# Performance work log

Measured on AMD Instinct MI355X. Metric: run time of the kernel, lower is better.

The kernel has to match this reference:

```python
import jax, jax.numpy as jnp
import numpy as np

H_DIM = 768
NUM_HEADS = 12
HEAD_DIM = H_DIM // NUM_HEADS
ROPE_BASE = 10000.0


def rope_cos_sin(seq_len, dim):
    inv_freq = 1.0 / (ROPE_BASE ** (jnp.arange(0, dim, 2, dtype=jnp.float32) / dim))
    t = jnp.arange(seq_len, dtype=jnp.float32)
    freqs = jnp.outer(t, inv_freq)              # [seq, dim/2]
    emb = jnp.concatenate([freqs, freqs], axis=-1)  # [seq, dim]
    return jnp.cos(emb), jnp.sin(emb)


def rotate_half(x):
    x1, x2 = jnp.split(x, 2, axis=-1)
    return jnp.concatenate([-x2, x1], axis=-1)


def setup_inputs() -> dict:
    key = jax.random.key(0)
    ks = jax.random.split(key, 9)
    s = 1.0 / np.sqrt(H_DIM)
    inp = {
        'x': jax.random.normal(ks[0], (2, 8, 1024, H_DIM), dtype=jnp.float32),
        'Wq': jax.random.normal(ks[1], (H_DIM, H_DIM), dtype=jnp.float32) * s,
        'bq': jnp.zeros((H_DIM,), dtype=jnp.float32),
        'Wk': jax.random.normal(ks[2], (H_DIM, H_DIM), dtype=jnp.float32) * s,
        'bk': jnp.zeros((H_DIM,), dtype=jnp.float32),
        'Wv': jax.random.normal(ks[3], (H_DIM, H_DIM), dtype=jnp.float32) * s,
        'bv': jnp.zeros((H_DIM,), dtype=jnp.float32),
        'Wo': jax.random.normal(ks[4], (H_DIM, H_DIM), dtype=jnp.float32) * s,
        'bo': jnp.zeros((H_DIM,), dtype=jnp.float32),
        'mask': jnp.ones((2, 8, 1, 1, 1024), dtype=jnp.int32),
    }
    return inp


def reference(x, Wq, bq, Wk, bk, Wv, bv, Wo, bo, mask):
    b, r, s, d = x.shape
    H, D = NUM_HEADS, HEAD_DIM

    def proj(W, bvec):
        # [b,r,s,d] -> [b,r,H,s,D]
        y = x @ W + bvec
        return y.reshape(b, r, s, H, D).transpose(0, 1, 3, 2, 4)

    q = proj(Wq, bq)
    k = proj(Wk, bk)
    v = proj(Wv, bv)

    cos, sin = rope_cos_sin(s, D)   # [s, D]
    cos = cos[None, None, None]     # broadcast over b,r,H
    sin = sin[None, None, None]
    q = q * cos + rotate_half(q) * sin
    k = k * cos + rotate_half(k) * sin

    scores = jnp.einsum('brhqd,brhkd->brhqk', q, k) / jnp.sqrt(jnp.float32(D))
    scores = jnp.where(mask == 0, -jnp.inf, scores)
    probs = jax.nn.softmax(scores, axis=-1)  # dropout is identity in eval
    out = jnp.einsum('brhqk,brhkd->brhqd', probs, v)
    out = out.transpose(0, 1, 3, 2, 4).reshape(b, r, s, d)
    return out @ Wo + bo
```

## Files before the change

kernel.cpp:

```cpp
#include <hip/hip_runtime.h>


#define M_TOT 16384
#define DM    768
#define NH    12
#define HD    64
#define SEQ   1024

typedef __attribute__((ext_vector_type(8))) __bf16 bf16x8;
typedef __attribute__((ext_vector_type(4))) __bf16 bf16x4;
typedef __attribute__((ext_vector_type(4))) short s16x4;
typedef __attribute__((ext_vector_type(4))) float  f32x4;

static __device__ __forceinline__ unsigned short f2b(float f) {
  unsigned u = __builtin_bit_cast(unsigned, f);
  u += 0x7FFFu + ((u >> 16) & 1u);
  return (unsigned short)(u >> 16);
}
static __device__ __forceinline__ float b2f(unsigned short s) {
  unsigned u = ((unsigned)s) << 16;
  return __builtin_bit_cast(float, u);
}
static __device__ __forceinline__ unsigned cvt_pk_bf16(float lo, float hi) {
  unsigned d;
  asm("v_cvt_pk_bf16_f32 %0, %1, %2" : "=v"(d) : "v"(lo), "v"(hi));
  return d;
}

static __device__ __forceinline__ f32x4 mfma16(uint2 a, uint2 b, f32x4 c) {
#if __has_builtin(__builtin_amdgcn_mfma_f32_16x16x16_bf16)
  union U { uint2 u; bf16x4 v; } A, B;
  A.u = a; B.u = b;
  return __builtin_amdgcn_mfma_f32_16x16x16_bf16(A.v, B.v, c, 0, 0, 0);
#else
  union U { uint2 u; s16x4 v; } A, B;
  A.u = a; B.u = b;
  return __builtin_amdgcn_mfma_f32_16x16x16bf16_1k(A.v, B.v, c, 0, 0, 0);
#endif
}

static __device__ __forceinline__ void gl_lds16(const void* g, void* l) {
  __builtin_amdgcn_global_load_lds(
      (const __attribute__((address_space(1))) unsigned*)g,
      (__attribute__((address_space(3))) unsigned*)l, 16, 0, 0);
}

static __device__ __forceinline__ int swz_src(int c) {
  return ((c >> 3) << 6) + (((c & 7) ^ ((c >> 3) & 7)) << 3);
}
static __device__ __forceinline__ int swz_rd(int row, int col16) {
  return (row << 6) + ((col16 ^ (row & 7)) << 3);
}

__global__ void cvt_x(const float* __restrict__ x, unsigned short* __restrict__ xb) {
  const int n4 = M_TOT * DM / 4;
  for (int i = blockIdx.x * blockDim.x + threadIdx.x; i < n4; i += gridDim.x * blockDim.x) {
    float4 v = ((const float4*)x)[i];
    ushort4 o;
    o.x = f2b(v.x); o.y = f2b(v.y); o.z = f2b(v.z); o.w = f2b(v.w);
    ((ushort4*)xb)[i] = o;
  }
}

__global__ void prep(const float* __restrict__ Wq, const float* __restrict__ Wk,
                     const float* __restrict__ Wv, const float* __restrict__ Wo,
                     unsigned short* __restrict__ Wt,
                     float* __restrict__ cosT, float* __restrict__ sinT,
                     const float* __restrict__ bq, const float* __restrict__ bk,
                     const float* __restrict__ bv, float* __restrict__ bcat) {
  __shared__ float T[64][65];
  const int bid = blockIdx.x;
  const int t = threadIdx.x;
  if (bid < 576) {
    const int wsel = bid / 144, r144 = bid % 144;
    const int k0 = (r144 % 12) * 64, n0 = (r144 / 12) * 64;
    const float* W = wsel == 0 ? Wq : wsel == 1 ? Wk : wsel == 2 ? Wv : Wo;
#pragma unroll
    for (int p = 0; p < 16; ++p) {
      int e = p * 256 + t, r = e >> 6, c = e & 63;
      T[r][c] = W[(size_t)(k0 + r) * DM + n0 + c];
    }
    __syncthreads();
    unsigned short* dst = Wt + (size_t)wsel * DM * DM;
#pragma unroll
    for (int p = 0; p < 16; ++p) {
      int e = p * 256 + t, r = e >> 6, c = e & 63;
      dst[(size_t)(n0 + r) * DM + k0 + c] = f2b(T[c][r]);
    }
  } else if (bid < 704) {
    int i = (bid - 576) * 256 + t;
    int s = i >> 5, j = i & 31;
    float inv = powf(10000.0f, -(float)j * (1.0f / 32.0f));
    float ang = (float)s * inv;
    cosT[i] = cosf(ang);
    sinT[i] = sinf(ang);
  } else {
    int i = (bid - 704) * 256 + t;
    if (i < 3 * DM)
      bcat[i] = i < DM ? bq[i] : (i < 2 * DM ? bk[i - DM] : bv[i - 2 * DM]);
  }
}

static __device__ __forceinline__ void gemm_core(const unsigned short* __restrict__ A,
                                                 const unsigned short* __restrict__ Bt,
                                                 int m0, int n0, f32x4 acc[4][4],
                                                 char* smem) {
  unsigned short* As = (unsigned short*)smem;
  unsigned short* Bs = As + 128 * 64;
  const int tid = threadIdx.x, lane = tid & 63, w = tid >> 6;
  const int wr = w >> 1, wc = w & 1;
  const int lr = lane & 15, g4 = lane >> 4;

#pragma unroll
  for (int i = 0; i < 4; ++i)
#pragma unroll
    for (int j = 0; j < 4; ++j) acc[i][j] = (f32x4){0.f, 0.f, 0.f, 0.f};

  auto STAGE = [&](int k0) {
#pragma unroll
    for (int p = 0; p < 4; ++p) {
      int cb = p * 256 + w * 64;
      int c = cb + lane;
      const int ro = c >> 3;
      const int co = ((c & 7) ^ (ro & 7)) << 3;
      gl_lds16(A + (size_t)(m0 + ro) * DM + k0 + co, (char*)As + cb * 16);
      gl_lds16(Bt + (size_t)(n0 + ro) * DM + k0 + co, (char*)Bs + cb * 16);
    }
  };

  STAGE(0);
  __syncthreads();

  for (int kt = 0; kt < DM / 64; ++kt) {
    bf16x8 a[4], b[4];
    {
      const int ch = g4;
#pragma unroll
      for (int i = 0; i < 4; ++i) {
        const int row = wr * 64 + i * 16 + lr;
        a[i] = *(const bf16x8*)&As[(row << 6) + ((ch ^ (row & 7)) << 3)];
      }
#pragma unroll
      for (int j = 0; j < 4; ++j) {
        const int row = wc * 64 + j * 16 + lr;
        b[j] = *(const bf16x8*)&Bs[(row << 6) + ((ch ^ (row & 7)) << 3)];
      }
      __builtin_amdgcn_s_setprio(1);
#pragma unroll
      for (int i = 0; i < 4; ++i)
#pragma unroll
        for (int j = 0; j < 4; ++j)
          acc[i][j] = __builtin_amdgcn_mfma_f32_16x16x32_bf16(a[i], b[j], acc[i][j], 0, 0, 0);
      __builtin_amdgcn_s_setprio(0);
    }
    bf16x8 a1[4], b1[4];
    {
      const int ch = 4 + g4;
#pragma unroll
      for (int i = 0; i < 4; ++i) {
        const int row = wr * 64 + i * 16 + lr;
        a1[i] = *(const bf16x8*)&As[(row << 6) + ((ch ^ (row & 7)) << 3)];
      }
#pragma unroll
      for (int j = 0; j < 4; ++j) {
        const int row = wc * 64 + j * 16 + lr;
        b1[j] = *(const bf16x8*)&Bs[(row << 6) + ((ch ^ (row & 7)) << 3)];
      }
    }
    __syncthreads();
    if (kt + 1 < DM / 64) STAGE((kt + 1) * 64);
    __builtin_amdgcn_s_setprio(1);
#pragma unroll
    for (int i = 0; i < 4; ++i)
#pragma unroll
      for (int j = 0; j < 4; ++j)
        acc[i][j] = __builtin_amdgcn_mfma_f32_16x16x32_bf16(a1[i], b1[j], acc[i][j], 0, 0, 0);
    __builtin_amdgcn_s_setprio(0);
    __syncthreads();
  }
}

__global__ __launch_bounds__(256, 4) void gemm_qkv(
    const unsigned short* __restrict__ xb, const unsigned short* __restrict__ Wt,
    const float* __restrict__ bcat, const float* __restrict__ cosT,
    const float* __restrict__ sinT, unsigned short* __restrict__ Qh,
    unsigned short* __restrict__ Kh, unsigned short* __restrict__ Vt) {
  __shared__ alignas(16) char smem[32768];
  const int id = blockIdx.x;
  const int xcdc = id & 7, rem = id >> 3;
  const int y = rem % 18, xc = rem / 18;
  const int xm = xc * 8 + xcdc;
  const int m0 = xm * 128, n0 = y * 128;
  f32x4 acc[4][4];
  gemm_core(xb, Wt, m0, n0, acc, smem);

  const int tid = threadIdx.x, lane = tid & 63, w = tid >> 6;
  const int wr = w >> 1, wc = w & 1;
  const int lr = lane & 15, g4 = lane >> 4;
  const int zone = y / 6;
  const int wcol0 = n0 - zone * DM + wc * 64;
  const int h = wcol0 >> 6;
  const int br = m0 >> 10;
  const int s_base = (m0 & 1023) + wr * 64;

  if (zone == 2) {
    unsigned short* dstb = Vt + ((size_t)(br * NH + h) * HD) * SEQ;
#pragma unroll
    for (int j = 0; j < 4; ++j) {
      const int d = j * 16 + lr;
      const float bv = bcat[n0 + wc * 64 + d];
#pragma unroll
      for (int i = 0; i < 4; ++i) {
        const int s0 = s_base + i * 16 + g4 * 4;
        ushort4 st;
        st.x = f2b(acc[i][j][0] + bv);
        st.y = f2b(acc[i][j][1] + bv);
        st.z = f2b(acc[i][j][2] + bv);
        st.w = f2b(acc[i][j][3] + bv);
        *(ushort4*)&dstb[(size_t)d * SEQ + s0] = st;
      }
    }
  } else {
    const float sc = zone == 0 ? 0.125f * 1.44269504f : 1.0f;
    unsigned short* dstb = (zone ? Kh : Qh) + ((size_t)(br * NH + h) * SEQ) * HD;
    char* Wb = smem + (size_t)w * 8192;
    const int s_q = s_base + lane;
    const int bcol = n0 + wc * 64;

#pragma unroll
    for (int hh = 0; hh < 2; ++hh) {
#pragma unroll
      for (int jj = 0; jj < 2; ++jj) {
        const int jp = hh + jj * 2;
        const float bv = bcat[bcol + jp * 16 + lr];
        const int dslot = jj * 16 + lr;
        const int sub = (dslot & 3) * 4;
        const int ch = dslot >> 2;
#pragma unroll
        for (int i = 0; i < 4; ++i) {
#pragma unroll
          for (int r = 0; r < 4; ++r) {
            const int s_loc = i * 16 + g4 * 4 + r;
            *(float*)(Wb + s_loc * 128 + ((ch ^ (s_loc & 7)) << 4) + sub) =
                (acc[i][jp][r] + bv) * sc;
          }
        }
      }
      unsigned short* drow = dstb + (size_t)s_q * HD + hh * 16;
      const char* Rb = Wb + lane * 128;
      const int lx = lane & 7;
#pragma unroll
      for (int c = 0; c < 4; ++c) {
        f32x4 va = *(const f32x4*)(Rb + ((c ^ lx) << 4));
        f32x4 vb = *(const f32x4*)(Rb + (((c + 4) ^ lx) << 4));
        float4 c4 = *(const float4*)&cosT[s_q * 32 + hh * 16 + c * 4];
        float4 s4 = *(const float4*)&sinT[s_q * 32 + hh * 16 + c * 4];
        uint2 oa, ob;
        oa.x = cvt_pk_bf16(va[0] * c4.x - vb[0] * s4.x, va[1] * c4.y - vb[1] * s4.y);
        oa.y = cvt_pk_bf16(va[2] * c4.z - vb[2] * s4.z, va[3] * c4.w - vb[3] * s4.w);
        ob.x = cvt_pk_bf16(vb[0] * c4.x + va[0] * s4.x, vb[1] * c4.y + va[1] * s4.y);
        ob.y = cvt_pk_bf16(vb[2] * c4.z + va[2] * s4.z, vb[3] * c4.w + va[3] * s4.w);
        *(uint2*)(drow + c * 4)      = oa;
        *(uint2*)(drow + 32 + c * 4) = ob;
      }
    }
  }
}

__global__ __launch_bounds__(256, 4) void gemm_o(const unsigned short* __restrict__ attnb,
                                                 const unsigned short* __restrict__ WtO,
                                                 const float* __restrict__ bo,
                                                 float* __restrict__ out) {
  __shared__ alignas(16) char smem[32768];
  const int id = blockIdx.x;
  const int xcdc = id & 7, rem = id >> 3;
  const int y = rem % 6, xc = rem / 6;
  const int m0 = (xc * 8 + xcdc) * 128, n0 = y * 128;
  f32x4 acc[4][4];
  gemm_core(attnb, WtO, m0, n0, acc, smem);
  const int tid = threadIdx.x, lane = tid & 63, w = tid >> 6;
  const int wr = w >> 1, wc = w & 1;
  const int lr = lane & 15, g4 = lane >> 4;
#pragma unroll
  for (int j = 0; j < 4; ++j) {
    const int col = n0 + wc * 64 + j * 16 + lr;
    const float bv = bo[col];
#pragma unroll
    for (int i = 0; i < 4; ++i) {
      const int rowb = m0 + wr * 64 + i * 16 + g4 * 4;
#pragma unroll
      for (int r = 0; r < 4; ++r)
        out[(size_t)(rowb + r) * DM + col] = acc[i][j][r] + bv;
    }
  }
}

__global__ __launch_bounds__(256) void attn_fwd(const unsigned short* __restrict__ Qh,
                                                const unsigned short* __restrict__ Kh,
                                                const unsigned short* __restrict__ Vt,
                                                const int* __restrict__ mask,
                                                unsigned short* __restrict__ attnb) {
  __shared__ unsigned short Ks[2][64 * 64];
  __shared__ unsigned short Vs[2][64 * 64];
  const int id = blockIdx.x;
  const int xcdc = id & 7, rem = id >> 3;
  const int qp = rem & 7, g = rem >> 3;
  const int brh = g * 8 + xcdc;
  const int br = brh / NH, h = brh - br * NH;
  const int tid = threadIdx.x, lane = tid & 63, w = tid >> 6;
  const int lr = lane & 15, g4 = lane >> 4;

  const unsigned short* Kg = Kh + (size_t)brh * SEQ * HD;
  const unsigned short* Vg = Vt + (size_t)brh * HD * SEQ;
  const int* mrow0 = mask + (size_t)br * SEQ + g4 * 4;

  int4 mi = *(const int4*)&mask[(size_t)br * SEQ + tid * 4];
  const int allLive = __syncthreads_and(mi.x && mi.y && mi.z && mi.w);

#pragma unroll
  for (int p = 0; p < 2; ++p) {
    int cb = p * 256 + w * 64;
    int c = cb + lane;
    gl_lds16(Kg + swz_src(c), (char*)Ks[0] + cb * 16);
    gl_lds16(Vg + (size_t)(c >> 3) * SEQ + (((c & 7) ^ ((c >> 3) & 7)) << 3),
             (char*)Vs[0] + cb * 16);
  }

  const unsigned short* Qg0 =
      Qh + ((size_t)brh * SEQ + qp * 128 + w * 16 + lr) * HD;
  bf16x8 qa0[2], qa1[2];
  qa0[0] = *(const bf16x8*)(Qg0 + g4 * 8);
  qa0[1] = *(const bf16x8*)(Qg0 + 32 + g4 * 8);
  qa1[0] = *(const bf16x8*)(Qg0 + (size_t)64 * HD + g4 * 8);
  qa1[1] = *(const bf16x8*)(Qg0 + (size_t)64 * HD + 32 + g4 * 8);

  f32x4 o0[4], o1[4], lacc0, lacc1;
#pragma unroll
  for (int j = 0; j < 4; ++j) {
    o0[j] = (f32x4){0.f, 0.f, 0.f, 0.f};
    o1[j] = (f32x4){0.f, 0.f, 0.f, 0.f};
  }
  lacc0 = (f32x4){0.f, 0.f, 0.f, 0.f};
  lacc1 = (f32x4){0.f, 0.f, 0.f, 0.f};
  const uint2 ones = {0x3F803F80u, 0x3F803F80u};

  __syncthreads();

  unsigned short* KsC = Ks[0];
  unsigned short* VsC = Vs[0];
  unsigned short* KsN = Ks[1];
  unsigned short* VsN = Vs[1];

  for (int kb = 0; kb < SEQ / 64; ++kb) {
    if (kb + 1 < SEQ / 64) {
#pragma unroll
      for (int p = 0; p < 2; ++p) {
        int cb = p * 256 + w * 64;
        int c = cb + lane;
        gl_lds16(Kg + (size_t)(kb + 1) * 64 * HD + swz_src(c), (char*)KsN + cb * 16);
        gl_lds16(Vg + (size_t)(c >> 3) * SEQ + (kb + 1) * 64 +
                     (((c & 7) ^ ((c >> 3) & 7)) << 3),
                 (char*)VsN + cb * 16);
      }
    }

#pragma unroll
    for (int qi = 0; qi < 2; ++qi) {
      const bf16x8* qa = qi ? qa1 : qa0;
      f32x4* o = qi ? o1 : o0;
      f32x4& lacc = qi ? lacc1 : lacc0;

      f32x4 s4[4];
#pragma unroll
      for (int j = 0; j < 4; ++j) s4[j] = (f32x4){0.f, 0.f, 0.f, 0.f};
      __builtin_amdgcn_s_setprio(1);
#pragma unroll
      for (int kk = 0; kk < 2; ++kk) {
#pragma unroll
        for (int j = 0; j < 4; ++j) {
          bf16x8 kf = *(const bf16x8*)&KsC[swz_rd(j * 16 + lr, kk * 4 + g4)];
          s4[j] = __builtin_amdgcn_mfma_f32_16x16x32_bf16(kf, qa[kk], s4[j], 0, 0, 0);
        }
      }
      __builtin_amdgcn_s_setprio(0);

      if (!allLive) {
        const int* mr = mrow0 + kb * 64;
#pragma unroll
        for (int j = 0; j < 4; ++j) {
          int4 mq = *(const int4*)&mr[j * 16];
          s4[j][0] += mq.x ? 0.f : -3e38f;
          s4[j][1] += mq.y ? 0.f : -3e38f;
          s4[j][2] += mq.z ? 0.f : -3e38f;
          s4[j][3] += mq.w ? 0.f : -3e38f;
        }
      }

      uint2 wb[4];
#pragma unroll
      for (int j = 0; j < 4; ++j) {
        wb[j].x = cvt_pk_bf16(exp2f(s4[j][0]), exp2f(s4[j][1]));
        wb[j].y = cvt_pk_bf16(exp2f(s4[j][2]), exp2f(s4[j][3]));
      }

      __builtin_amdgcn_s_setprio(1);
#pragma unroll
      for (int j = 0; j < 4; ++j) lacc = mfma16(ones, wb[j], lacc);
#pragma unroll
      for (int jj = 0; jj < 4; ++jj) {
        const int row = jj * 16 + lr;
#pragma unroll
        for (int j = 0; j < 4; ++j) {
          const int c8 = j * 4 + g4;
          uint2 av = *(const uint2*)&VsC[(row << 6) + ((((c8 >> 1) ^ (lr & 7))) << 3) +
                                         ((c8 & 1) << 2)];
          o[jj] = mfma16(av, wb[j], o[jj]);
        }
      }
      __builtin_amdgcn_s_setprio(0);
    }

    __syncthreads();
    unsigned short* t;
    t = KsC; KsC = KsN; KsN = t;
    t = VsC; VsC = VsN; VsN = t;
  }

#pragma unroll
  for (int qi = 0; qi < 2; ++qi) {
    f32x4* o = qi ? o1 : o0;
    float l = qi ? lacc1[0] : lacc0[0];
    float inv = l > 0.f ? 1.0f / l : 0.f;
    unsigned short* dst =
        attnb + ((size_t)(br * SEQ + qp * 128 + qi * 64 + w * 16 + lr)) * DM + h * HD;
#pragma unroll
    for (int j = 0; j < 4; ++j) {
      ushort4 st;
      st.x = f2b(o[j][0] * inv);
      st.y = f2b(o[j][1] * inv);
      st.z = f2b(o[j][2] * inv);
      st.w = f2b(o[j][3] * inv);
      *(ushort4*)&dst[j * 16 + g4 * 4] = st;
    }
  }
}

extern "C" void kernel_launch(void* const* d_in, const int* in_sizes, int n_in,
                              void* d_out, int out_size, void* d_ws, size_t ws_size,
                              hipStream_t stream) {
  const float* x  = (const float*)d_in[0];
  const float* Wq = (const float*)d_in[1];
  const float* bq = (const float*)d_in[2];
  const float* Wk = (const float*)d_in[3];
  const float* bk = (const float*)d_in[4];
  const float* Wv = (const float*)d_in[5];
  const float* bv = (const float*)d_in[6];
  const float* Wo = (const float*)d_in[7];
  const float* bo = (const float*)d_in[8];
  const int* mask = (const int*)d_in[9];
  float* out = (float*)d_out;

  const size_t OFF_XB   = 0;
  const size_t OFF_WT   = 25165824;
  const size_t OFF_COS  = 29884416;
  const size_t OFF_SIN  = 30015488;
  const size_t OFF_BC   = 30146560;
  const size_t OFF_ATT  = 30158848;
  const size_t OFF_QH   = 55324672;
  const size_t OFF_KH   = 80490496;
  const size_t OFF_VT   = 105656320;
  const size_t REQUIRED = 130822144;
  if (ws_size < REQUIRED) return;

  char* w = (char*)d_ws;
  unsigned short* xb   = (unsigned short*)(w + OFF_XB);
  unsigned short* Wt   = (unsigned short*)(w + OFF_WT);
  float* cosT          = (float*)(w + OFF_COS);
  float* sinT          = (float*)(w + OFF_SIN);
  float* bcat          = (float*)(w + OFF_BC);
  unsigned short* attnb = (unsigned short*)(w + OFF_ATT);
  unsigned short* Qh   = (unsigned short*)(w + OFF_QH);
  unsigned short* Kh   = (unsigned short*)(w + OFF_KH);
  unsigned short* Vt   = (unsigned short*)(w + OFF_VT);

  cvt_x<<<2048, 256, 0, stream>>>(x, xb);
  prep<<<713, 256, 0, stream>>>(Wq, Wk, Wv, Wo, Wt, cosT, sinT, bq, bk, bv, bcat);
  gemm_qkv<<<2304, 256, 0, stream>>>(xb, Wt, bcat, cosT, sinT, Qh, Kh, Vt);
  attn_fwd<<<1536, 256, 0, stream>>>(Qh, Kh, Vt, mask, attnb);
  gemm_o<<<768, 256, 0, stream>>>(attnb, Wt + (size_t)3 * DM * DM, bo, out);
}
```

Baseline: 231.0 us.

## Single-buffer K tile and interleave both query sub-tiles per key fragment

The attention kernel now computes QK^T for both 64-row query sub-tiles in one pass, so each K fragment read from LDS feeds two MFMAs and each V fragment is shared by both output accumulators. Because the K tile is fully consumed before the mid-loop barrier, K is reduced from a double buffer to a single buffer and the next K/V prefetch is issued after that barrier. This halves K/V LDS reads and cuts LDS footprint. In exchange it raises register pressure from two live score and weight sets, and adds a second barrier per iteration that shortens the window for prefetch overlap.

```diff
diff --git a/kernel.cpp b/kernel.cpp
--- a/kernel.cpp
+++ b/kernel.cpp
@@ -300,7 +300,7 @@
                                                 const unsigned short* __restrict__ Vt,
                                                 const int* __restrict__ mask,
                                                 unsigned short* __restrict__ attnb) {
-  __shared__ unsigned short Ks[2][64 * 64];
+  __shared__ unsigned short Ks[64 * 64];
   __shared__ unsigned short Vs[2][64 * 64];
   const int id = blockIdx.x;
   const int xcdc = id & 7, rem = id >> 3;
@@ -321,7 +321,7 @@
   for (int p = 0; p < 2; ++p) {
     int cb = p * 256 + w * 64;
     int c = cb + lane;
-    gl_lds16(Kg + swz_src(c), (char*)Ks[0] + cb * 16);
+    gl_lds16(Kg + swz_src(c), (char*)Ks + cb * 16);
     gl_lds16(Vg + (size_t)(c >> 3) * SEQ + (((c & 7) ^ ((c >> 3) & 7)) << 3),
              (char*)Vs[0] + cb * 16);
   }
@@ -346,84 +346,87 @@
 
   __syncthreads();
 
-  unsigned short* KsC = Ks[0];
   unsigned short* VsC = Vs[0];
-  unsigned short* KsN = Ks[1];
   unsigned short* VsN = Vs[1];
 
   for (int kb = 0; kb < SEQ / 64; ++kb) {
+    f32x4 s40[4], s41[4];
+#pragma unroll
+    for (int j = 0; j < 4; ++j) {
+      s40[j] = (f32x4){0.f, 0.f, 0.f, 0.f};
+      s41[j] = (f32x4){0.f, 0.f, 0.f, 0.f};
+    }
+    __builtin_amdgcn_s_setprio(1);
+#pragma unroll
+    for (int kk = 0; kk < 2; ++kk) {
+#pragma unroll
+      for (int j = 0; j < 4; ++j) {
+        bf16x8 kf = *(const bf16x8*)&Ks[swz_rd(j * 16 + lr, kk * 4 + g4)];
+        s40[j] = __builtin_amdgcn_mfma_f32_16x16x32_bf16(kf, qa0[kk], s40[j], 0, 0, 0);
+        s41[j] = __builtin_amdgcn_mfma_f32_16x16x32_bf16(kf, qa1[kk], s41[j], 0, 0, 0);
+      }
+    }
+    __builtin_amdgcn_s_setprio(0);
+
+    __syncthreads();
+
     if (kb + 1 < SEQ / 64) {
 #pragma unroll
       for (int p = 0; p < 2; ++p) {
         int cb = p * 256 + w * 64;
         int c = cb + lane;
-        gl_lds16(Kg + (size_t)(kb + 1) * 64 * HD + swz_src(c), (char*)KsN + cb * 16);
+        gl_lds16(Kg + (size_t)(kb + 1) * 64 * HD + swz_src(c), (char*)Ks + cb * 16);
         gl_lds16(Vg + (size_t)(c >> 3) * SEQ + (kb + 1) * 64 +
                      (((c & 7) ^ ((c >> 3) & 7)) << 3),
                  (char*)VsN + cb * 16);
       }
     }
 
-#pragma unroll
-    for (int qi = 0; qi < 2; ++qi) {
-      const bf16x8* qa = qi ? qa1 : qa0;
-      f32x4* o = qi ? o1 : o0;
-      f32x4& lacc = qi ? lacc1 : lacc0;
-
-      f32x4 s4[4];
-#pragma unroll
-      for (int j = 0; j < 4; ++j) s4[j] = (f32x4){0.f, 0.f, 0.f, 0.f};
-      __builtin_amdgcn_s_setprio(1);
-#pragma unroll
-      for (int kk = 0; kk < 2; ++kk) {
-#pragma unroll
-        for (int j = 0; j < 4; ++j) {
-          bf16x8 kf = *(const bf16x8*)&KsC[swz_rd(j * 16 + lr, kk * 4 + g4)];
-          s4[j] = __builtin_amdgcn_mfma_f32_16x16x32_bf16(kf, qa[kk], s4[j], 0, 0, 0);
-        }
-      }
-      __builtin_amdgcn_s_setprio(0);
-
-      if (!allLive) {
-        const int* mr = mrow0 + kb * 64;
-#pragma unroll
-        for (int j = 0; j < 4; ++j) {
-          int4 mq = *(const int4*)&mr[j * 16];
-          s4[j][0] += mq.x ? 0.f : -3e38f;
-          s4[j][1] += mq.y ? 0.f : -3e38f;
-          s4[j][2] += mq.z ? 0.f : -3e38f;
-          s4[j][3] += mq.w ? 0.f : -3e38f;
-        }
-      }
-
-      uint2 wb[4];
+    if (!allLive) {
+      const int* mr = mrow0 + kb * 64;
 #pragma unroll
       for (int j = 0; j < 4; ++j) {
-        wb[j].x = cvt_pk_bf16(exp2f(s4[j][0]), exp2f(s4[j][1]));
-        wb[j].y = cvt_pk_bf16(exp2f(s4[j][2]), exp2f(s4[j][3]));
-      }
-
-      __builtin_amdgcn_s_setprio(1);
-#pragma unroll
-      for (int j = 0; j < 4; ++j) lacc = mfma16(ones, wb[j], lacc);
-#pragma unroll
-      for (int jj = 0; jj < 4; ++jj) {
-        const int row = jj * 16 + lr;
-#pragma unroll
-        for (int j = 0; j < 4; ++j) {
-          const int c8 = j * 4 + g4;
-          uint2 av = *(const uint2*)&VsC[(row << 6) + ((((c8 >> 1) ^ (lr & 7))) << 3) +
-                                         ((c8 & 1) << 2)];
-          o[jj] = mfma16(av, wb[j], o[jj]);
-        }
-      }
-      __builtin_amdgcn_s_setprio(0);
-    }
+        int4 mq = *(const int4*)&mr[j * 16];
+        float m0f = mq.x ? 0.f : -3e38f;
+        float m1f = mq.y ? 0.f : -3e38f;
+        float m2f = mq.z ? 0.f : -3e38f;
+        float m3f = mq.w ? 0.f : -3e38f;
+        s40[j][0] += m0f; s40[j][1] += m1f; s40[j][2] += m2f; s40[j][3] += m3f;
+        s41[j][0] += m0f; s41[j][1] += m1f; s41[j][2] += m2f; s41[j][3] += m3f;
+      }
+    }
+
+    uint2 wb0[4], wb1[4];
+#pragma unroll
+    for (int j = 0; j < 4; ++j) {
+      wb0[j].x = cvt_pk_bf16(exp2f(s40[j][0]), exp2f(s40[j][1]));
+      wb0[j].y = cvt_pk_bf16(exp2f(s40[j][2]), exp2f(s40[j][3]));
+      wb1[j].x = cvt_pk_bf16(exp2f(s41[j][0]), exp2f(s41[j][1]));
+      wb1[j].y = cvt_pk_bf16(exp2f(s41[j][2]), exp2f(s41[j][3]));
+    }
+
+    __builtin_amdgcn_s_setprio(1);
+#pragma unroll
+    for (int j = 0; j < 4; ++j) {
+      lacc0 = mfma16(ones, wb0[j], lacc0);
+      lacc1 = mfma16(ones, wb1[j], lacc1);
+    }
+#pragma unroll
+    for (int jj = 0; jj < 4; ++jj) {
+      const int row = jj * 16 + lr;
+#pragma unroll
+      for (int j = 0; j < 4; ++j) {
+        const int c8 = j * 4 + g4;
+        uint2 av = *(const uint2*)&VsC[(row << 6) + ((((c8 >> 1) ^ (lr & 7))) << 3) +
+                                       ((c8 & 1) << 2)];
+        o0[jj] = mfma16(av, wb0[j], o0[jj]);
+        o1[jj] = mfma16(av, wb1[j], o1[jj]);
+      }
+    }
+    __builtin_amdgcn_s_setprio(0);
 
     __syncthreads();
-    unsigned short* t;
-    t = KsC; KsC = KsN; KsN = t;
-    t = VsC; VsC = VsN; VsN = t;
+    unsigned short* t = VsC; VsC = VsN; VsN = t;
   }
 
 #pragma unroll
```

After: 234.8 us. No clear change (+1.6%).
